# Optimization experiments

Measured on AMD Instinct MI355X. Metric: run time of the kernel, lower is better.

The kernel has to match this reference:

```python
import jax, jax.numpy as jnp
import numpy as np

D_MODEL = 1024
NHEAD = 16
HEAD_DIM = D_MODEL // NHEAD
B, S = 4, 2048


def setup_inputs() -> dict:
    key = jax.random.key(0)
    ks = jax.random.split(key, 10)
    scale = 1.0 / np.sqrt(D_MODEL)
    inp = {
        "x": jax.random.normal(ks[0], (B, S, D_MODEL), dtype=jnp.float32),
        "y": jax.random.normal(ks[1], (B, S, D_MODEL), dtype=jnp.float32),
        "wq": jax.random.normal(ks[2], (D_MODEL, D_MODEL), dtype=jnp.float32) * scale,
        "bq": jnp.zeros((D_MODEL,), dtype=jnp.float32),
        "wk": jax.random.normal(ks[3], (D_MODEL, D_MODEL), dtype=jnp.float32) * scale,
        "bk": jnp.zeros((D_MODEL,), dtype=jnp.float32),
        "wv": jax.random.normal(ks[4], (D_MODEL, D_MODEL), dtype=jnp.float32) * scale,
        "bv": jnp.zeros((D_MODEL,), dtype=jnp.float32),
        "wo": jax.random.normal(ks[5], (D_MODEL, D_MODEL), dtype=jnp.float32) * scale,
        "bo": jnp.zeros((D_MODEL,), dtype=jnp.float32),
    }
    return inp


def reference(x, y, wq, bq, wk, bk, wv, bv, wo, bo):
    # Linear projections (torch nn.Linear: x @ W.T + b; here weights stored as [in, out])
    q = x @ wq + bq  # [B, S, D]
    k = y @ wk + bk
    v = y @ wv + bv
    # split heads -> [B, H, S, Dh]
    def heads(t):
        return t.reshape(B, S, NHEAD, HEAD_DIM).transpose(0, 2, 1, 3)
    q, k, v = heads(q), heads(k), heads(v)
    scores = jnp.einsum("bhqd,bhkd->bhqk", q, k) / jnp.sqrt(jnp.float32(HEAD_DIM))
    attn = jax.nn.softmax(scores, axis=-1)  # dropout = identity in eval mode
    out = jnp.einsum("bhqk,bhkd->bhqd", attn, v)
    out = out.transpose(0, 2, 1, 3).reshape(B, S, D_MODEL)
    return out @ wo + bo
```

## Files before the change

### kernel.cpp

```cpp
#include <hip/hip_runtime.h>
#include <stdint.h>

#define D_MODEL 1024
#define NHEAD 16
#define HEAD_DIM 64
#define BATCH 4
#define SEQ 2048
#define ROWS (BATCH*SEQ)

typedef __attribute__((ext_vector_type(8))) short short8;
typedef __attribute__((ext_vector_type(4))) float f32x4;
typedef __attribute__((ext_vector_type(2))) unsigned int u32x2;
typedef unsigned short u16;
typedef unsigned int u32;

#define QSCALE 0.18033688011112042f

__device__ __forceinline__ u16 f2b(float f) {
  union { float f; uint32_t u; } in; in.f = f;
  uint32_t u = in.u;
  return (u16)((u + 0x7FFFu + ((u >> 16) & 1u)) >> 16);
}

__device__ __forceinline__ void async_lds16(const void* g, void* l) {
  __builtin_amdgcn_global_load_lds(
      (const __attribute__((address_space(1))) uint32_t*)g,
      (__attribute__((address_space(3))) uint32_t*)l,
      16, 0, 0);
}

__device__ __forceinline__ u32 pack_bf16(float lo, float hi) {
  union { float f; uint32_t u; } a, b; a.f = lo; b.f = hi;
  return __builtin_amdgcn_perm(b.u + 0x8000u, a.u + 0x8000u, 0x07060302u);
}

__global__ void __launch_bounds__(256) cvt_kernel(const float* __restrict__ x,
                                                  const float* __restrict__ y,
                                                  u16* __restrict__ xb,
                                                  u16* __restrict__ yb) {
  const float* in = blockIdx.y ? y : x;
  u16* out = blockIdx.y ? yb : xb;
  int i = blockIdx.x * 256 + threadIdx.x;
  float4 v = ((const float4*)in)[i];
  ushort4 o;
  o.x = f2b(v.x); o.y = f2b(v.y); o.z = f2b(v.z); o.w = f2b(v.w);
  ((ushort4*)out)[i] = o;
}

__global__ void __launch_bounds__(256) wtrans_kernel(const float* __restrict__ wq,
                                                     const float* __restrict__ wk,
                                                     const float* __restrict__ wv,
                                                     const float* __restrict__ wo,
                                                     u16* __restrict__ wtbase) {
  __shared__ u16 tile[64 * 65];
  int z = blockIdx.z;
  const float* w = (z == 0) ? wq : (z == 1 ? wk : (z == 2 ? wv : wo));
  u16* wt = wtbase + (size_t)z * D_MODEL * D_MODEL;
  int t = threadIdx.x;
  int c = t & 63, rb = t >> 6;
  int k0 = blockIdx.x * 64, n0 = blockIdx.y * 64;
#pragma unroll
  for (int i = 0; i < 16; ++i) {
    int r = rb + i * 4;
    tile[c * 65 + r] = f2b(w[(size_t)(k0 + r) * D_MODEL + n0 + c]);
  }
  __syncthreads();
#pragma unroll
  for (int i = 0; i < 16; ++i) {
    int r = rb + i * 4;
    wt[(size_t)(n0 + r) * D_MODEL + k0 + c] = tile[r * 65 + c];
  }
}

template <int MODE>
__device__ __forceinline__ void gemm_bt_core(const u16* __restrict__ A,
                                             const u16* __restrict__ Bt,
                                             const float* __restrict__ bias,
                                             void* __restrict__ Cout, float scale,
                                             int m0, int n0) {
  constexpr int K = 1024, N = 1024;
  constexpr bool SWAP = (MODE != 2);
  __shared__ u16 As[2][128 * 32];
  __shared__ u16 Bs[2][128 * 32];
  int tid = threadIdx.x;
  int wave = tid >> 6, lane = tid & 63;
  int quad = lane >> 4, l16 = lane & 15;
  int wm = wave & 1, wn = wave >> 1;

  f32x4 acc[4][4];
#pragma unroll
  for (int p = 0; p < 4; ++p)
#pragma unroll
    for (int q = 0; q < 4; ++q) acc[p][q] = f32x4{0.f, 0.f, 0.f, 0.f};

  int srow = lane >> 2;
  int scol = (lane & 3) * 16;

  for (int k0 = 0; k0 < K; k0 += 64) {
#pragma unroll
    for (int kh = 0; kh < 2; ++kh) {
#pragma unroll
      for (int i = 0; i < 2; ++i) {
        int c = wave * 2 + i;
        const char* ga = (const char*)(A + (size_t)(m0 + c * 16 + srow) * K + k0 + kh * 32) + scol;
        async_lds16(ga, (char*)As[kh] + c * 1024);
        const char* gb = (const char*)(Bt + (size_t)(n0 + c * 16 + srow) * K + k0 + kh * 32) + scol;
        async_lds16(gb, (char*)Bs[kh] + c * 1024);
      }
    }
    __syncthreads();

#pragma unroll
    for (int kh = 0; kh < 2; ++kh) {
      short8 fa[4], fb[4];
#pragma unroll
      for (int p = 0; p < 4; ++p)
        fa[p] = SWAP
          ? *(const short8*)(Bs[kh] + (wn * 64 + p * 16 + l16) * 32 + quad * 8)
          : *(const short8*)(As[kh] + (wm * 64 + p * 16 + l16) * 32 + quad * 8);
#pragma unroll
      for (int q = 0; q < 4; ++q)
        fb[q] = SWAP
          ? *(const short8*)(As[kh] + (wm * 64 + q * 16 + l16) * 32 + quad * 8)
          : *(const short8*)(Bs[kh] + (wn * 64 + q * 16 + l16) * 32 + quad * 8);
#pragma unroll
      for (int p = 0; p < 4; ++p)
#pragma unroll
        for (int q = 0; q < 4; ++q)
          acc[p][q] = __builtin_amdgcn_mfma_f32_16x16x32_bf16(fa[p], fb[q], acc[p][q], 0, 0, 0);
    }
    __syncthreads();
  }

  if (MODE == 2) {
    int sblk = n0 + wn * 64;
    int bb = sblk >> 11;
    int ssb = sblk & 2047;
#pragma unroll
    for (int p = 0; p < 4; ++p) {
      int dbase = m0 + wm * 64 + p * 16 + quad * 4;
      float4 b4 = *(const float4*)(bias + dbase);
#pragma unroll
      for (int r = 0; r < 4; ++r) {
        int d = dbase + r;
        float bv = ((const float*)&b4)[r];
        u32 lo = pack_bf16(acc[p][0][r] + bv, acc[p][1][r] + bv);
        u32 hi = pack_bf16(acc[p][2][r] + bv, acc[p][3][r] + bv);
        size_t vtrow = ((size_t)bb * 16 + (d >> 6)) * 64 + (d & 63);
        *(u32x2*)((u16*)Cout + vtrow * 2048 + ssb + 4 * l16) = u32x2{lo, hi};
      }
    }
  } else {
#pragma unroll
    for (int p = 0; p < 4; ++p) {
      int nbase = n0 + wn * 64 + p * 16 + quad * 4;
      float4 b4 = *(const float4*)(bias + nbase);
#pragma unroll
      for (int q = 0; q < 4; ++q) {
        size_t mrow = (size_t)(m0 + wm * 64 + q * 16 + l16);
        float v0 = (acc[p][q][0] + b4.x) * scale;
        float v1 = (acc[p][q][1] + b4.y) * scale;
        float v2 = (acc[p][q][2] + b4.z) * scale;
        float v3 = (acc[p][q][3] + b4.w) * scale;
        if (MODE == 1) {
          *(f32x4*)((float*)Cout + mrow * N + nbase) = f32x4{v0, v1, v2, v3};
        } else {
          *(u32x2*)((u16*)Cout + mrow * N + nbase) = u32x2{pack_bf16(v0, v1), pack_bf16(v2, v3)};
        }
      }
    }
  }
}

__global__ void __launch_bounds__(256, 4) gemm_qkv_kernel(
    const u16* __restrict__ xb, const u16* __restrict__ yb,
    const u16* __restrict__ wqT, const u16* __restrict__ wkT, const u16* __restrict__ wvT,
    const float* __restrict__ bq, const float* __restrict__ bk, const float* __restrict__ bv,
    u16* __restrict__ q, u16* __restrict__ k, u16* __restrict__ vt) {
  int bx = blockIdx.x, z = blockIdx.y;
  if (z == 0) {
    gemm_bt_core<0>(xb, wqT, bq, q, QSCALE, (bx >> 3) * 128, (bx & 7) * 128);
  } else if (z == 1) {
    gemm_bt_core<0>(yb, wkT, bk, k, 1.0f, (bx >> 3) * 128, (bx & 7) * 128);
  } else {
    gemm_bt_core<2>(wvT, yb, bv, vt, 1.0f, (bx & 7) * 128, (bx >> 3) * 128);
  }
}

__global__ void __launch_bounds__(256, 4) gemm_o_kernel(const u16* __restrict__ ao,
                                                        const u16* __restrict__ woT,
                                                        const float* __restrict__ bo,
                                                        float* __restrict__ out) {
  gemm_bt_core<1>(ao, woT, bo, out, 1.0f, blockIdx.y * 128, blockIdx.x * 128);
}

__global__ void __launch_bounds__(256, 4) attn_kernel(const u16* __restrict__ Q,
                                                      const u16* __restrict__ Kp,
                                                      const u16* __restrict__ Vt,
                                                      u16* __restrict__ Outp) {
  __shared__ u16 Ks[64 * 64];
  __shared__ u16 Vts[64 * 64];
  __shared__ u16 Ps[4][32 * 64];

  int tid = threadIdx.x, wave = tid >> 6, lane = tid & 63;
  int quad = lane >> 4, l16 = lane & 15;
  int bh = blockIdx.x;
  int b = bh >> 4, h = bh & 15;
  int q0 = blockIdx.y * 128 + wave * 32;
  size_t gbase = (size_t)b * SEQ * D_MODEL;
  const u16* kbase = Kp + gbase + (size_t)h * HEAD_DIM;
  const u16* vbase = Vt + (size_t)bh * HEAD_DIM * SEQ;
  const u16* qrow = Q + gbase + (size_t)q0 * D_MODEL + (size_t)h * HEAD_DIM;

  short8 aq[2][2];
#pragma unroll
  for (int rs = 0; rs < 2; ++rs)
#pragma unroll
    for (int dc = 0; dc < 2; ++dc)
      aq[rs][dc] = *(const short8*)(qrow + (size_t)(rs * 16 + l16) * D_MODEL + dc * 32 + quad * 8);

  f32x4 Oacc[2][4];
  float lpart[2][4];
#pragma unroll
  for (int rs = 0; rs < 2; ++rs)
#pragma unroll
    for (int ni = 0; ni < 4; ++ni) Oacc[rs][ni] = f32x4{0.f, 0.f, 0.f, 0.f};
#pragma unroll
  for (int rs = 0; rs < 2; ++rs)
#pragma unroll
    for (int r = 0; r < 4; ++r) lpart[rs][r] = 0.f;

  size_t koff[2], voff[2];
  int dstoff[2];
#pragma unroll
  for (int i = 0; i < 2; ++i) {
    int c = i * 256 + tid;
    int krow = c >> 3, kgp = c & 7;
    koff[i] = (size_t)krow * D_MODEL + (size_t)((kgp ^ (krow & 7)) * 8);
    voff[i] = (size_t)krow * SEQ + (size_t)((kgp ^ (krow & 7)) * 8);
    dstoff[i] = i * 4096 + wave * 1024;
  }

  for (int kv0 = 0; kv0 < SEQ; kv0 += 64) {
    __syncthreads();
#pragma unroll
    for (int i = 0; i < 2; ++i) {
      async_lds16(kbase + (size_t)kv0 * D_MODEL + koff[i], (char*)Ks + dstoff[i]);
      async_lds16(vbase + (size_t)kv0 + voff[i], (char*)Vts + dstoff[i]);
    }
    __syncthreads();

    u16* Pw = Ps[wave];
    int x = l16 & 7;

    short8 kf[4][2];
#pragma unroll
    for (int sub = 0; sub < 4; ++sub) {
      const u16* kr = Ks + (sub * 16 + l16) * 64;
      kf[sub][0] = *(const short8*)(kr + ((quad ^ x) << 3));
      kf[sub][1] = *(const short8*)(kr + (((4 + quad) ^ x) << 3));
    }

#pragma unroll
    for (int rs = 0; rs < 2; ++rs) {
      f32x4 S[4];
#pragma unroll
      for (int sub = 0; sub < 4; ++sub) {
        f32x4 s = f32x4{0.f, 0.f, 0.f, 0.f};
        s = __builtin_amdgcn_mfma_f32_16x16x32_bf16(aq[rs][0], kf[sub][0], s, 0, 0, 0);
        s = __builtin_amdgcn_mfma_f32_16x16x32_bf16(aq[rs][1], kf[sub][1], s, 0, 0, 0);
        S[sub] = s;
      }
#pragma unroll
      for (int r = 0; r < 4; ++r) {
        float p0 = __builtin_amdgcn_exp2f(S[0][r]);
        float p1 = __builtin_amdgcn_exp2f(S[1][r]);
        float p2 = __builtin_amdgcn_exp2f(S[2][r]);
        float p3 = __builtin_amdgcn_exp2f(S[3][r]);
        lpart[rs][r] += (p0 + p1) + (p2 + p3);
        u32 lo = pack_bf16(p0, p1);
        u32 hi = pack_bf16(p2, p3);
        int row = rs * 16 + quad * 4 + r;
        int off = row * 64 + (((l16 >> 1) ^ (row & 7)) << 3) + ((l16 & 1) << 2);
        *(u32x2*)(Pw + off) = u32x2{lo, hi};
      }
    }

#pragma unroll
    for (int kc = 0; kc < 2; ++kc) {
      short8 pa[2];
#pragma unroll
      for (int rs = 0; rs < 2; ++rs) {
        int prow = rs * 16 + l16;
        pa[rs] = *(const short8*)(Pw + prow * 64 + ((((kc << 2) + quad) ^ x) << 3));
      }
#pragma unroll
      for (int ni = 0; ni < 4; ++ni) {
        int d = ni * 16 + l16;
        short8 bv = *(const short8*)(Vts + d * 64 + ((((kc << 2) + quad) ^ (l16 & 7)) << 3));
        Oacc[0][ni] = __builtin_amdgcn_mfma_f32_16x16x32_bf16(pa[0], bv, Oacc[0][ni], 0, 0, 0);
        Oacc[1][ni] = __builtin_amdgcn_mfma_f32_16x16x32_bf16(pa[1], bv, Oacc[1][ni], 0, 0, 0);
      }
    }
  }

#pragma unroll
  for (int rs = 0; rs < 2; ++rs)
#pragma unroll
    for (int r = 0; r < 4; ++r) {
      float l = lpart[rs][r];
      l += __shfl_xor(l, 1);
      l += __shfl_xor(l, 2);
      l += __shfl_xor(l, 4);
      l += __shfl_xor(l, 8);
      float inv = 1.0f / l;
      size_t orow = gbase + (size_t)(q0 + rs * 16 + quad * 4 + r) * D_MODEL + (size_t)h * HEAD_DIM;
#pragma unroll
      for (int ni = 0; ni < 4; ++ni)
        Outp[orow + ni * 16 + l16] = f2b(Oacc[rs][ni][r] * inv);
    }
}

extern "C" void kernel_launch(void* const* d_in, const int* in_sizes, int n_in,
                              void* d_out, int out_size, void* d_ws, size_t ws_size,
                              hipStream_t stream) {
  const float* x  = (const float*)d_in[0];
  const float* y  = (const float*)d_in[1];
  const float* wq = (const float*)d_in[2];
  const float* bq = (const float*)d_in[3];
  const float* wk = (const float*)d_in[4];
  const float* bk = (const float*)d_in[5];
  const float* wv = (const float*)d_in[6];
  const float* bv = (const float*)d_in[7];
  const float* wo = (const float*)d_in[8];
  const float* bo = (const float*)d_in[9];
  float* out = (float*)d_out;

  char* ws = (char*)d_ws;
  const size_t SZ_ACT = (size_t)ROWS * D_MODEL * 2;
  const size_t SZ_W   = (size_t)D_MODEL * D_MODEL * 2;
  u16* xb  = (u16*)(ws);
  u16* yb  = (u16*)(ws + SZ_ACT);
  u16* wT  = (u16*)(ws + 2 * SZ_ACT);
  u16* wqT = wT;
  u16* wkT = (u16*)(ws + 2 * SZ_ACT + SZ_W);
  u16* wvT = (u16*)(ws + 2 * SZ_ACT + 2 * SZ_W);
  u16* woT = (u16*)(ws + 2 * SZ_ACT + 3 * SZ_W);
  u16* qb  = (u16*)(ws + 2 * SZ_ACT + 4 * SZ_W);
  u16* kb  = (u16*)(ws + 3 * SZ_ACT + 4 * SZ_W);
  u16* vt  = (u16*)(ws + 4 * SZ_ACT + 4 * SZ_W);
  u16* ao  = (u16*)(ws + 5 * SZ_ACT + 4 * SZ_W);

  cvt_kernel<<<dim3(8192, 2), 256, 0, stream>>>(x, y, xb, yb);
  wtrans_kernel<<<dim3(16, 16, 4), 256, 0, stream>>>(wq, wk, wv, wo, wT);
  gemm_qkv_kernel<<<dim3(512, 3), 256, 0, stream>>>(xb, yb, wqT, wkT, wvT, bq, bk, bv, qb, kb, vt);
  attn_kernel<<<dim3(64, 16), 256, 0, stream>>>(qb, kb, vt, ao);
  gemm_o_kernel<<<dim3(8, 64), 256, 0, stream>>>(ao, woT, bo, out);
}
```

Before: 329.8 us.

## Double-buffer K/V tiles in attention and shrink per-wave P scratch

The attention kernel now keeps two LDS buffers for the K and V tiles. It issues the async loads for the next tile before computing on the current one, so global-memory latency overlaps the MFMA and softmax work, and it drops one barrier per iteration. The per-wave P scratch shrinks to 16 rows, and each row-strip's P fragments are read back right after they are written, which keeps total LDS growth modest. In exchange LDS per block rises, which could limit occupancy. Correctness relies on the remaining barrier also waiting for the earlier async loads to finish.

```diff
diff --git a/kernel.cpp b/kernel.cpp
--- a/kernel.cpp
+++ b/kernel.cpp
@@ -198,9 +198,9 @@
                                                       const u16* __restrict__ Kp,
                                                       const u16* __restrict__ Vt,
                                                       u16* __restrict__ Outp) {
-  __shared__ u16 Ks[64 * 64];
-  __shared__ u16 Vts[64 * 64];
-  __shared__ u16 Ps[4][32 * 64];
+  __shared__ u16 Ks[2][64 * 64];
+  __shared__ u16 Vts[2][64 * 64];
+  __shared__ u16 Ps[4][16 * 64];
 
   int tid = threadIdx.x, wave = tid >> 6, lane = tid & 63;
   int quad = lane >> 4, l16 = lane & 15;
@@ -241,26 +241,39 @@
     dstoff[i] = i * 4096 + wave * 1024;
   }
 
-  for (int kv0 = 0; kv0 < SEQ; kv0 += 64) {
+#pragma unroll
+  for (int i = 0; i < 2; ++i) {
+    async_lds16(kbase + koff[i], (char*)Ks[0] + dstoff[i]);
+    async_lds16(vbase + voff[i], (char*)Vts[0] + dstoff[i]);
+  }
+
+  constexpr int NT = SEQ / 64;
+  for (int t = 0; t < NT; ++t) {
+    int cur = t & 1;
     __syncthreads();
-#pragma unroll
-    for (int i = 0; i < 2; ++i) {
-      async_lds16(kbase + (size_t)kv0 * D_MODEL + koff[i], (char*)Ks + dstoff[i]);
-      async_lds16(vbase + (size_t)kv0 + voff[i], (char*)Vts + dstoff[i]);
-    }
-    __syncthreads();
-
+    if (t + 1 < NT) {
+      size_t kvoff = (size_t)(t + 1) * 64;
+#pragma unroll
+      for (int i = 0; i < 2; ++i) {
+        async_lds16(kbase + kvoff * D_MODEL + koff[i], (char*)Ks[cur ^ 1] + dstoff[i]);
+        async_lds16(vbase + kvoff + voff[i], (char*)Vts[cur ^ 1] + dstoff[i]);
+      }
+    }
+
+    const u16* Kc = Ks[cur];
+    const u16* Vc = Vts[cur];
     u16* Pw = Ps[wave];
     int x = l16 & 7;
 
     short8 kf[4][2];
 #pragma unroll
     for (int sub = 0; sub < 4; ++sub) {
-      const u16* kr = Ks + (sub * 16 + l16) * 64;
+      const u16* kr = Kc + (sub * 16 + l16) * 64;
       kf[sub][0] = *(const short8*)(kr + ((quad ^ x) << 3));
       kf[sub][1] = *(const short8*)(kr + (((4 + quad) ^ x) << 3));
     }
 
+    short8 pa[2][2];
 #pragma unroll
     for (int rs = 0; rs < 2; ++rs) {
       f32x4 S[4];
@@ -280,26 +293,23 @@
         lpart[rs][r] += (p0 + p1) + (p2 + p3);
         u32 lo = pack_bf16(p0, p1);
         u32 hi = pack_bf16(p2, p3);
-        int row = rs * 16 + quad * 4 + r;
+        int row = quad * 4 + r;
         int off = row * 64 + (((l16 >> 1) ^ (row & 7)) << 3) + ((l16 & 1) << 2);
         *(u32x2*)(Pw + off) = u32x2{lo, hi};
       }
+#pragma unroll
+      for (int kc = 0; kc < 2; ++kc)
+        pa[rs][kc] = *(const short8*)(Pw + l16 * 64 + ((((kc << 2) + quad) ^ x) << 3));
     }
 
 #pragma unroll
     for (int kc = 0; kc < 2; ++kc) {
-      short8 pa[2];
-#pragma unroll
-      for (int rs = 0; rs < 2; ++rs) {
-        int prow = rs * 16 + l16;
-        pa[rs] = *(const short8*)(Pw + prow * 64 + ((((kc << 2) + quad) ^ x) << 3));
-      }
 #pragma unroll
       for (int ni = 0; ni < 4; ++ni) {
         int d = ni * 16 + l16;
-        short8 bv = *(const short8*)(Vts + d * 64 + ((((kc << 2) + quad) ^ (l16 & 7)) << 3));
-        Oacc[0][ni] = __builtin_amdgcn_mfma_f32_16x16x32_bf16(pa[0], bv, Oacc[0][ni], 0, 0, 0);
-        Oacc[1][ni] = __builtin_amdgcn_mfma_f32_16x16x32_bf16(pa[1], bv, Oacc[1][ni], 0, 0, 0);
+        short8 bv = *(const short8*)(Vc + d * 64 + ((((kc << 2) + quad) ^ (l16 & 7)) << 3));
+        Oacc[0][ni] = __builtin_amdgcn_mfma_f32_16x16x32_bf16(pa[0][kc], bv, Oacc[0][ni], 0, 0, 0);
+        Oacc[1][ni] = __builtin_amdgcn_mfma_f32_16x16x32_bf16(pa[1][kc], bv, Oacc[1][ni], 0, 0, 0);
       }
     }
   }
```

Result: no change. 327.6 us (-0.7%).
